# Performance work log

Hardware: AMD Instinct MI355X
Metric: run time of the kernel (lower is better)

Reference implementation:

```python
import jax, jax.numpy as jnp
import numpy as np
from jax import lax

B, C, H, W = 16, 1, 1024, 1024
BOUNDARY_WEIGHT = 3.0
# two iterations of a flat 5x5 structuring element == one flat 9x9 window
WIN = 9
PAD = WIN // 2


def setup_inputs() -> dict:
    key = jax.random.key(0)
    k1, k2, k3, k4 = jax.random.split(key, 4)
    logits = jax.random.normal(k1, (B, C, H, W), dtype=jnp.float32)
    # spatially-coherent binary masks (random disks), mimicking car masks
    cy = jax.random.uniform(k2, (B,), minval=0.3 * H, maxval=0.7 * H)
    cx = jax.random.uniform(k3, (B,), minval=0.3 * W, maxval=0.7 * W)
    r = jax.random.uniform(k4, (B,), minval=0.15 * H, maxval=0.4 * H)
    ys = jnp.arange(H, dtype=jnp.float32)
    xs = jnp.arange(W, dtype=jnp.float32)
    d2 = (ys[None, :, None] - cy[:, None, None]) ** 2 + (xs[None, None, :] - cx[:, None, None]) ** 2
    targets = (d2 < (r[:, None, None] ** 2)).astype(jnp.float32)[:, None]  # [B,1,H,W]
    return {"logits": logits, "targets": targets}


def _morph(t, op, init):
    # flat-SE morphology over HxW via reduce_window; cv2 default border is
    # the neutral value for the op, matching init padding.
    return lax.reduce_window(
        t, init, op,
        window_dimensions=(1, 1, WIN, WIN),
        window_strides=(1, 1, 1, 1),
        padding=[(0, 0), (0, 0), (PAD, PAD), (PAD, PAD)],
    )


def reference(logits, targets):
    dilated = _morph(targets, lax.max, -jnp.inf)
    eroded = _morph(targets, lax.min, jnp.inf)
    boundary = dilated - eroded  # 1 on mask boundary band, else 0
    weights = 1.0 + (BOUNDARY_WEIGHT - 1.0) * boundary
    # stable BCE-with-logits: max(x,0) - x*y + log1p(exp(-|x|))
    x, y = logits, targets
    per_elem = jnp.maximum(x, 0.0) - x * y + jax.nn.softplus(-jnp.abs(x))
    return jnp.mean(weights * per_elem)
```

## Files before the change

kernel.cpp:

```cpp
#include <hip/hip_runtime.h>

#define BATCH 16
#define IMG_H 1024
#define IMG_W 1024
#define WORDS 16
#define TOTAL_PX (BATCH * IMG_H * IMG_W)
#define TOTAL_WORDS (TOTAL_PX / 64)
typedef unsigned long long u64;
typedef float f32x4 __attribute__((ext_vector_type(4)));

__device__ __forceinline__ float bce1(float x, bool y)
{
    unsigned xu = __float_as_uint(x);
    float sgn = __uint_as_float(xu ^ (y ? 0x80000000u : 0u));
    float a   = __uint_as_float(xu & 0x7fffffffu);
    float t   = __builtin_exp2f(a * -1.44269504088896340736f);
    float l2  = __builtin_log2f(1.0f + t);
    return fmaf(l2, 0.69314718055994530942f, fmaxf(sgn, 0.0f));
}

__device__ __forceinline__ u64 spread4(u64 x)
{
    x = (x | (x << 24)) & 0x000000FF000000FFull;
    x = (x | (x << 12)) & 0x000F000F000F000Full;
    x = (x | (x << 6))  & 0x0303030303030303ull;
    x = (x | (x << 3))  & 0x1111111111111111ull;
    return x;
}

#define A_NT 256
#define A_WPB (A_NT / 64)
#define A_BLOCKS (TOTAL_PX / 512 / A_WPB)

__global__ __launch_bounds__(A_NT, 8)
void wbce_main_kernel(const float* __restrict__ logits,
                      const float* __restrict__ targets,
                      u64* __restrict__ pak,
                      float* __restrict__ partial)
{
    __shared__ float sRed[A_WPB];
    const int tid = threadIdx.x, lane = tid & 63, wv = tid >> 6;
    const int gw = blockIdx.x * A_WPB + wv;
    const size_t basePx = (size_t)gw * 512;
    const float* tpl = targets + basePx + lane * 4;
    const float* lpl = logits  + basePx + lane * 4;

    f32x4 t0, t1, x0, x1;
    asm volatile(
        "global_load_dwordx4 %0, %4, off\n\t"
        "global_load_dwordx4 %1, %4, off offset:1024\n\t"
        "global_load_dwordx4 %2, %5, off\n\t"
        "global_load_dwordx4 %3, %5, off offset:1024"
        : "=&v"(t0), "=&v"(t1), "=&v"(x0), "=&v"(x1)
        : "v"(tpl), "v"(lpl));

    asm volatile("s_waitcnt vmcnt(2)" : "+v"(t0), "+v"(t1));

    u64 b00 = __ballot(t0.x > 0.5f), b01 = __ballot(t0.y > 0.5f);
    u64 b02 = __ballot(t0.z > 0.5f), b03 = __ballot(t0.w > 0.5f);
    u64 b10 = __ballot(t1.x > 0.5f), b11 = __ballot(t1.y > 0.5f);
    u64 b12 = __ballot(t1.z > 0.5f), b13 = __ballot(t1.w > 0.5f);

    {
        const int c = (lane >> 2) & 1;
        const unsigned sh = (lane & 3) * 16u;
        u64 e0 = c ? b10 : b00, e1 = c ? b11 : b01;
        u64 e2 = c ? b12 : b02, e3 = c ? b13 : b03;
        u64 word =  spread4((e0 >> sh) & 0xFFFFu)
                 | (spread4((e1 >> sh) & 0xFFFFu) << 1)
                 | (spread4((e2 >> sh) & 0xFFFFu) << 2)
                 | (spread4((e3 >> sh) & 0xFFFFu) << 3);
        if (lane < 8) pak[(size_t)gw * 8 + lane] = word;
    }

    asm volatile("s_waitcnt vmcnt(0)" : "+v"(x0), "+v"(x1));

    float acc = bce1(x0.x, t0.x > 0.5f) + bce1(x0.y, t0.y > 0.5f)
              + bce1(x0.z, t0.z > 0.5f) + bce1(x0.w, t0.w > 0.5f)
              + bce1(x1.x, t1.x > 0.5f) + bce1(x1.y, t1.y > 0.5f)
              + bce1(x1.z, t1.z > 0.5f) + bce1(x1.w, t1.w > 0.5f);

    #pragma unroll
    for (int off = 32; off > 0; off >>= 1)
        acc += __shfl_down(acc, off, 64);
    if (lane == 0) sRed[wv] = acc;
    __syncthreads();
    if (tid == 0) {
        float s = 0.0f;
        #pragma unroll
        for (int i = 0; i < A_WPB; ++i) s += sRed[i];
        partial[blockIdx.x] = s;
    }
}

#define B_NT 256
__global__ __launch_bounds__(B_NT, 8)
void wbce_morph_kernel(const float* __restrict__ logits,
                       const u64* __restrict__ pak,
                       float* __restrict__ partial2)
{
    __shared__ float sRed[B_NT / 64];
    const int tid = threadIdx.x, lane = tid & 63, wv = tid >> 6;
    const int idx = blockIdx.x * B_NT + tid;
    const int w   = idx & 15;
    const int row = (idx >> 4) & (IMG_H - 1);
    const int img = idx >> 14;
    const u64* ib = pak + (size_t)img * (IMG_H * WORDS);

    u64 d = 0ULL, e = ~0ULL, Cw = 0ULL;
    const int r0 = row >= 4 ? row - 4 : 0;
    const int r1 = row <= IMG_H - 5 ? row + 4 : IMG_H - 1;
    for (int r = r0; r <= r1; ++r) {
        const u64* rp = ib + (size_t)r * WORDS;
        u64 c  = rp[w];
        u64 P  = (w > 0)  ? rp[w - 1] : 0ULL;
        u64 N  = (w < 15) ? rp[w + 1] : 0ULL;
        u64 Pe = (w > 0)  ? P : ~0ULL;
        u64 Ne = (w < 15) ? N : ~0ULL;
        u64 hd = c, he = c;
        #pragma unroll
        for (int s = 1; s <= 4; ++s) {
            hd |= (c >> s) | (N  << (64 - s));
            hd |= (c << s) | (P  >> (64 - s));
            he &= (c >> s) | (Ne << (64 - s));
            he &= (c << s) | (Pe >> (64 - s));
        }
        d |= hd;
        e &= he;
        if (r == row) Cw = c;
    }
    u64 bnd = d & ~e;

    float acc = 0.0f;
    u64 act_mask = __ballot(bnd != 0ULL);
    const int wavebase = blockIdx.x * B_NT + wv * 64;
    while (act_mask) {
        int s = __builtin_ctzll(act_mask);
        act_mask &= act_mask - 1;
        u64 bs = __shfl(bnd, s, 64);
        u64 cs = __shfl(Cw,  s, 64);
        if ((bs >> lane) & 1ULL) {
            float x = logits[((size_t)(wavebase + s) << 6) + lane];
            acc += 2.0f * bce1(x, ((cs >> lane) & 1ULL) != 0ULL);
        }
    }

    #pragma unroll
    for (int off = 32; off > 0; off >>= 1)
        acc += __shfl_down(acc, off, 64);
    if (lane == 0) sRed[wv] = acc;
    __syncthreads();
    if (tid == 0) {
        float s = 0.0f;
        #pragma unroll
        for (int i = 0; i < B_NT / 64; ++i) s += sRed[i];
        partial2[blockIdx.x] = s;
    }
}

#define D_NT 1024
__global__ __launch_bounds__(D_NT, 1)
void wbce_final_kernel(const float* __restrict__ partial,
                       const float* __restrict__ partial2,
                       float* __restrict__ out)
{
    __shared__ float sRed[D_NT / 64];
    const int tid = threadIdx.x;
    const float4* p4 = (const float4*)partial;
    float4 a = p4[tid];
    float4 b = p4[tid + D_NT];
    float acc = (a.x + a.y) + (a.z + a.w) + (b.x + b.y) + (b.z + b.w)
              + partial2[tid];
    #pragma unroll
    for (int off = 32; off > 0; off >>= 1)
        acc += __shfl_down(acc, off, 64);
    if ((tid & 63) == 0) sRed[tid >> 6] = acc;
    __syncthreads();
    if (tid == 0) {
        float s = 0.0f;
        #pragma unroll
        for (int i = 0; i < D_NT / 64; ++i) s += sRed[i];
        out[0] = s * (1.0f / 16777216.0f);
    }
}

extern "C" void kernel_launch(void* const* d_in, const int* in_sizes, int n_in,
                              void* d_out, int out_size, void* d_ws, size_t ws_size,
                              hipStream_t stream) {
    const float* logits  = (const float*)d_in[0];
    const float* targets = (const float*)d_in[1];
    float* out = (float*)d_out;

    char* ws = (char*)d_ws;
    u64*   pak      = (u64*)ws;
    float* partial  = (float*)(ws + (2u << 20));
    float* partial2 = (float*)(ws + (2u << 20) + 32768);

    wbce_main_kernel<<<dim3(A_BLOCKS), dim3(A_NT), 0, stream>>>(
        logits, targets, pak, partial);

    wbce_morph_kernel<<<dim3(TOTAL_WORDS / B_NT), dim3(B_NT), 0, stream>>>(
        logits, pak, partial2);

    wbce_final_kernel<<<dim3(1), dim3(D_NT), 0, stream>>>(partial, partial2, out);
}
```

Measured before the change: 44.34 us.

## Process four chunks per wave with double-buffered loads and direct ballot packing

The main kernel now has each wave handle 2048 pixels in four stages, double-buffering the register loads so the next chunk's loads are in flight while the current one is consumed. Targets are loaded one dword per lane, so each ballot directly yields a row-contiguous 64-bit mask word. This removes the spread4 bit interleaving, and lane 0 writes the words with vector stores. Logit bits are fetched by lane-dependent selection of the ballot results. The grid shrinks fourfold, the final reduction reads fewer partials, and occupancy bounds drop to 5, trading parallelism for memory-level overlap.

```diff
diff --git a/kernel.cpp b/kernel.cpp
--- a/kernel.cpp
+++ b/kernel.cpp
@@ -19,20 +19,36 @@
     return fmaf(l2, 0.69314718055994530942f, fmaxf(sgn, 0.0f));
 }
 
-__device__ __forceinline__ u64 spread4(u64 x)
-{
-    x = (x | (x << 24)) & 0x000000FF000000FFull;
-    x = (x | (x << 12)) & 0x000F000F000F000Full;
-    x = (x | (x << 6))  & 0x0303030303030303ull;
-    x = (x | (x << 3))  & 0x1111111111111111ull;
-    return x;
-}
-
 #define A_NT 256
 #define A_WPB (A_NT / 64)
-#define A_BLOCKS (TOTAL_PX / 512 / A_WPB)
-
-__global__ __launch_bounds__(A_NT, 8)
+#define A_BLOCKS (TOTAL_PX / 2048 / A_WPB)
+
+#define ISSUE(t, x0, x1, tp, lp)                                   \
+    asm volatile(                                                  \
+        "global_load_dword %0, %10, off\n\t"                       \
+        "global_load_dword %1, %10, off offset:256\n\t"            \
+        "global_load_dword %2, %10, off offset:512\n\t"            \
+        "global_load_dword %3, %10, off offset:768\n\t"            \
+        "global_load_dword %4, %10, off offset:1024\n\t"           \
+        "global_load_dword %5, %10, off offset:1280\n\t"           \
+        "global_load_dword %6, %10, off offset:1536\n\t"           \
+        "global_load_dword %7, %10, off offset:1792\n\t"           \
+        "global_load_dwordx4 %8, %11, off\n\t"                     \
+        "global_load_dwordx4 %9, %11, off offset:1024"             \
+        : "=&v"(t[0]), "=&v"(t[1]), "=&v"(t[2]), "=&v"(t[3]),      \
+          "=&v"(t[4]), "=&v"(t[5]), "=&v"(t[6]), "=&v"(t[7]),      \
+          "=&v"(x0), "=&v"(x1)                                     \
+        : "v"(tp), "v"(lp))
+
+#define WAIT_T(n, t)                                               \
+    asm volatile("s_waitcnt vmcnt(" #n ")"                         \
+        : "+v"(t[0]), "+v"(t[1]), "+v"(t[2]), "+v"(t[3]),          \
+          "+v"(t[4]), "+v"(t[5]), "+v"(t[6]), "+v"(t[7]))
+
+#define WAIT_X(n, x0, x1)                                          \
+    asm volatile("s_waitcnt vmcnt(" #n ")" : "+v"(x0), "+v"(x1))
+
+__global__ __launch_bounds__(A_NT, 5)
 void wbce_main_kernel(const float* __restrict__ logits,
                       const float* __restrict__ targets,
                       u64* __restrict__ pak,
@@ -41,44 +57,61 @@
     __shared__ float sRed[A_WPB];
     const int tid = threadIdx.x, lane = tid & 63, wv = tid >> 6;
     const int gw = blockIdx.x * A_WPB + wv;
-    const size_t basePx = (size_t)gw * 512;
-    const float* tpl = targets + basePx + lane * 4;
-    const float* lpl = logits  + basePx + lane * 4;
-
-    f32x4 t0, t1, x0, x1;
-    asm volatile(
-        "global_load_dwordx4 %0, %4, off\n\t"
-        "global_load_dwordx4 %1, %4, off offset:1024\n\t"
-        "global_load_dwordx4 %2, %5, off\n\t"
-        "global_load_dwordx4 %3, %5, off offset:1024"
-        : "=&v"(t0), "=&v"(t1), "=&v"(x0), "=&v"(x1)
-        : "v"(tpl), "v"(lpl));
-
-    asm volatile("s_waitcnt vmcnt(2)" : "+v"(t0), "+v"(t1));
-
-    u64 b00 = __ballot(t0.x > 0.5f), b01 = __ballot(t0.y > 0.5f);
-    u64 b02 = __ballot(t0.z > 0.5f), b03 = __ballot(t0.w > 0.5f);
-    u64 b10 = __ballot(t1.x > 0.5f), b11 = __ballot(t1.y > 0.5f);
-    u64 b12 = __ballot(t1.z > 0.5f), b13 = __ballot(t1.w > 0.5f);
-
-    {
-        const int c = (lane >> 2) & 1;
-        const unsigned sh = (lane & 3) * 16u;
-        u64 e0 = c ? b10 : b00, e1 = c ? b11 : b01;
-        u64 e2 = c ? b12 : b02, e3 = c ? b13 : b03;
-        u64 word =  spread4((e0 >> sh) & 0xFFFFu)
-                 | (spread4((e1 >> sh) & 0xFFFFu) << 1)
-                 | (spread4((e2 >> sh) & 0xFFFFu) << 2)
-                 | (spread4((e3 >> sh) & 0xFFFFu) << 3);
-        if (lane < 8) pak[(size_t)gw * 8 + lane] = word;
-    }
-
-    asm volatile("s_waitcnt vmcnt(0)" : "+v"(x0), "+v"(x1));
-
-    float acc = bce1(x0.x, t0.x > 0.5f) + bce1(x0.y, t0.y > 0.5f)
-              + bce1(x0.z, t0.z > 0.5f) + bce1(x0.w, t0.w > 0.5f)
-              + bce1(x1.x, t1.x > 0.5f) + bce1(x1.y, t1.y > 0.5f)
-              + bce1(x1.z, t1.z > 0.5f) + bce1(x1.w, t1.w > 0.5f);
+    const size_t basePx = (size_t)gw * 2048;
+    const float* tp0 = targets + basePx + lane;
+    const float* lp0 = logits  + basePx + lane * 4;
+
+    float tA[8], tB[8];
+    f32x4 xA0, xA1, xB0, xB1;
+    float acc = 0.0f;
+
+    #define STAGE_CONSUME(t, x0, x1, it)                                     \
+    do {                                                                     \
+        u64 b0 = __ballot(t[0] > 0.5f), b1 = __ballot(t[1] > 0.5f);          \
+        u64 b2 = __ballot(t[2] > 0.5f), b3 = __ballot(t[3] > 0.5f);          \
+        u64 b4 = __ballot(t[4] > 0.5f), b5 = __ballot(t[5] > 0.5f);          \
+        u64 b6 = __ballot(t[6] > 0.5f), b7 = __ballot(t[7] > 0.5f);          \
+            \
+        u64 w0 = (lane & 32) ? ((lane & 16) ? b3 : b2)                       \
+                             : ((lane & 16) ? b1 : b0);                      \
+        u64 w1 = (lane & 32) ? ((lane & 16) ? b7 : b6)                       \
+                             : ((lane & 16) ? b5 : b4);                      \
+        const unsigned sh = (lane & 15) * 4u;                                \
+        unsigned yb0 = (unsigned)(w0 >> sh) & 0xFu;                          \
+        unsigned yb1 = (unsigned)(w1 >> sh) & 0xFu;                          \
+        acc += bce1(x0.x, yb0 & 1u) + bce1(x0.y, yb0 & 2u)                   \
+             + bce1(x0.z, yb0 & 4u) + bce1(x0.w, yb0 & 8u)                   \
+             + bce1(x1.x, yb1 & 1u) + bce1(x1.y, yb1 & 2u)                   \
+             + bce1(x1.z, yb1 & 4u) + bce1(x1.w, yb1 & 8u);                  \
+        if (lane == 0) {                                                     \
+            ulonglong2* q = (ulonglong2*)(pak + (size_t)gw * 32 + (it) * 8); \
+            q[0] = make_ulonglong2(b0, b1);                                  \
+            q[1] = make_ulonglong2(b2, b3);                                  \
+            q[2] = make_ulonglong2(b4, b5);                                  \
+            q[3] = make_ulonglong2(b6, b7);                                  \
+        }                                                                    \
+    } while (0)
+
+    ISSUE(tA, xA0, xA1, tp0,        lp0);
+    ISSUE(tB, xB0, xB1, tp0 + 512,  lp0 + 512);
+
+    WAIT_T(12, tA);
+    WAIT_X(10, xA0, xA1);
+    STAGE_CONSUME(tA, xA0, xA1, 0);
+    ISSUE(tA, xA0, xA1, tp0 + 1024, lp0 + 1024);
+
+    WAIT_T(12, tB);
+    WAIT_X(10, xB0, xB1);
+    STAGE_CONSUME(tB, xB0, xB1, 1);
+    ISSUE(tB, xB0, xB1, tp0 + 1536, lp0 + 1536);
+
+    WAIT_T(12, tA);
+    WAIT_X(10, xA0, xA1);
+    STAGE_CONSUME(tA, xA0, xA1, 2);
+
+    WAIT_T(2, tB);
+    WAIT_X(0, xB0, xB1);
+    STAGE_CONSUME(tB, xB0, xB1, 3);
 
     #pragma unroll
     for (int off = 32; off > 0; off >>= 1)
@@ -166,11 +199,11 @@
 {
     __shared__ float sRed[D_NT / 64];
     const int tid = threadIdx.x;
-    const float4* p4 = (const float4*)partial;
-    float4 a = p4[tid];
-    float4 b = p4[tid + D_NT];
-    float acc = (a.x + a.y) + (a.z + a.w) + (b.x + b.y) + (b.z + b.w)
-              + partial2[tid];
+    float acc = partial2[tid];
+    if (tid < 512) {
+        float4 a = ((const float4*)partial)[tid];
+        acc += (a.x + a.y) + (a.z + a.w);
+    }
     #pragma unroll
     for (int off = 32; off > 0; off >>= 1)
         acc += __shfl_down(acc, off, 64);
@@ -194,7 +227,7 @@
     char* ws = (char*)d_ws;
     u64*   pak      = (u64*)ws;
     float* partial  = (float*)(ws + (2u << 20));
-    float* partial2 = (float*)(ws + (2u << 20) + 32768);
+    float* partial2 = (float*)(ws + (2u << 20) + 8192);
 
     wbce_main_kernel<<<dim3(A_BLOCKS), dim3(A_NT), 0, stream>>>(
         logits, targets, pak, partial);
```

Measured after the change: 46.01 us. 3.8% more time.
